# Kernel optimization log

Hardware: AMD Instinct MI355X
Metric: run time of the kernel (lower is better)

The kernel has to match this reference:

```python
import jax, jax.numpy as jnp
import numpy as np

B, N, IN_DIM, HIDDEN, N_CLASS = 32768, 25, 3, 128, 2

# BODY_25 skeleton edges from the repo
_SRC = np.array([17, 15, 18, 16, 0, 2, 3, 4, 5, 6, 7, 8, 9, 12, 10, 13, 11, 14, 23, 22, 24, 20, 19, 21])
_DST = np.array([15, 0, 16, 0, 1, 1, 2, 3, 1, 5, 6, 1, 8, 8, 9, 12, 10, 13, 22, 11, 11, 19, 14, 14])


def setup_inputs() -> dict:
    key = jax.random.key(0)
    ks = jax.random.split(key, 4)
    # skeleton edges + self loops (dgl.add_self_loop)
    src = jnp.asarray(np.concatenate([_SRC, np.arange(N)]), dtype=jnp.int64)
    dst = jnp.asarray(np.concatenate([_DST, np.arange(N)]), dtype=jnp.int64)
    return {
        "x": jax.random.normal(ks[0], (B, N, IN_DIM), dtype=jnp.float32),
        "src": src,
        "dst": dst,
        "W1": jax.random.normal(ks[1], (IN_DIM, HIDDEN), dtype=jnp.float32) / np.sqrt(IN_DIM),
        "b1": jnp.zeros((HIDDEN,), jnp.float32),
        "W2": jax.random.normal(ks[2], (HIDDEN, HIDDEN), dtype=jnp.float32) / np.sqrt(HIDDEN),
        "b2": jnp.zeros((HIDDEN,), jnp.float32),
        "Wfc": jax.random.normal(ks[3], (HIDDEN, N_CLASS), dtype=jnp.float32) / np.sqrt(HIDDEN),
        "bfc": jnp.zeros((N_CLASS,), jnp.float32),
    }


def reference(x, src, dst, W1, b1, W2, b2, Wfc, bfc):
    # x: [B, N, F] node features for B identical-topology skeleton graphs
    Bn, Nn, _ = x.shape
    ones = jnp.ones(src.shape, x.dtype)
    deg_out = jax.ops.segment_sum(ones, src, num_segments=Nn)  # [N]
    deg_in = jax.ops.segment_sum(ones, dst, num_segments=Nn)   # [N]
    # DGL GraphConv norm='both': D_in^{-1/2} A D_out^{-1/2} X W + b
    cs = jnp.where(deg_out > 0, deg_out ** -0.5, 0.0)
    ci = jnp.where(deg_in > 0, deg_in ** -0.5, 0.0)

    def gconv(h, W, b):
        msg = h[:, src, :] * cs[src][None, :, None]            # gather + src norm
        agg = jnp.zeros_like(h).at[:, dst, :].add(msg)          # scatter-add
        agg = agg * ci[None, :, None]                           # dst norm
        return agg @ W + b

    h = jax.nn.relu(gconv(x, W1, b1))
    h = jax.nn.relu(gconv(h, W2, b2))
    pooled = jnp.mean(h, axis=1)  # dgl.mean_nodes -> [B, HIDDEN]
    return pooled @ Wfc + bfc      # [B, N_CLASS]
```

## Files before the change

kernel.cpp:

```cpp
#include <hip/hip_runtime.h>

#define NN    25
#define FIN   3
#define HID   128
#define GPB   4
#define ROWDW 64

typedef int i32x4 __attribute__((ext_vector_type(4)));
typedef unsigned int uint;

static __device__ __forceinline__ long pack8(const int* q)
{
    unsigned long v = 0;
    #pragma unroll
    for (int j = 0; j < 8; ++j)
        v |= ((unsigned long)(unsigned char)(q[j] & 255)) << (8 * j);
    return (long)v;
}

__global__ void pack_w2_i8(const float* __restrict__ W2, float* __restrict__ scales,
                           long* __restrict__ w2q)
{
    __shared__ float red[4];
    const int tid = threadIdx.x;

    float m = 1e-20f;
    #pragma unroll
    for (int i = 0; i < (HID * HID) / 256; ++i)
        m = fmaxf(m, fabsf(W2[i * 256 + tid]));
    #pragma unroll
    for (int off = 32; off > 0; off >>= 1)
        m = fmaxf(m, __shfl_xor(m, off));
    if ((tid & 63) == 0) red[tid >> 6] = m;
    __syncthreads();
    const float bmax = fmaxf(fmaxf(red[0], red[1]), fmaxf(red[2], red[3]));
    const float Sb = 32000.0f / bmax;
    if (blockIdx.x == 0 && tid == 0) { scales[0] = bmax; scales[1] = Sb; }

    int gi = blockIdx.x * 256 + tid;
    int l  = gi & 63;
    int nt = (gi >> 6) & 7;
    int kt = (gi >> 9) & 3;
    int p  = gi >> 11;
    int n  = nt * 16 + (l & 15);
    int kb = kt * 32 + (l >> 4) * 8;
    int q8[8];
    #pragma unroll
    for (int j = 0; j < 8; ++j) {
        int qv = (int)rintf(W2[(kb + j) * HID + n] * Sb);
        qv = min(max(qv, -32600), 32600);
        int lo = ((qv + 128) & 255) - 128;
        int hi = (qv - lo) >> 8;
        q8[j] = p ? lo : hi;
    }
    w2q[gi] = pack8(q8);
}

static __device__ __forceinline__ void agg25_inplace(float2* A)
{
    const float cA = 0.40824829f;
    const float cB = 0.31622777f;
    const float cC = 0.44721360f;
    const float cH = 0.5f;
    const float cS = 0.70710678f;
    A[1]  = cB * (A[0] + A[2] + A[5] + A[8]) + cC * A[1];
    A[0]  = cA * (A[15] + A[16] + A[0]);
    A[2]  = cH * (A[3]  + A[2]);
    A[3]  = cH * (A[4]  + A[3]);
    A[4]  = cS *  A[4];
    A[5]  = cH * (A[6]  + A[5]);
    A[6]  = cH * (A[7]  + A[6]);
    A[7]  = cS *  A[7];
    A[8]  = cA * (A[9] + A[12] + A[8]);
    A[9]  = cH * (A[10] + A[9]);
    A[10] = cH * (A[11] + A[10]);
    A[11] = cA * (A[22] + A[24] + A[11]);
    A[12] = cH * (A[13] + A[12]);
    A[13] = cH * (A[14] + A[13]);
    A[14] = cA * (A[19] + A[21] + A[14]);
    A[15] = cH * (A[17] + A[15]);
    A[16] = cH * (A[18] + A[16]);
    A[17] = cS *  A[17];
    A[18] = cS *  A[18];
    A[19] = cH * (A[20] + A[19]);
    A[20] = cS *  A[20];
    A[21] = cS *  A[21];
    A[22] = cH * (A[23] + A[22]);
    A[23] = cS *  A[23];
    A[24] = cS *  A[24];
}

static __device__ __forceinline__ void unpack16(uint4 d, long& hi, long& lo)
{
    uint h01 = __builtin_amdgcn_perm(d.y, d.x, 0x07050301u) ^ 0x80808080u;
    uint h23 = __builtin_amdgcn_perm(d.w, d.z, 0x07050301u) ^ 0x80808080u;
    uint l01 = __builtin_amdgcn_perm(d.y, d.x, 0x06040200u) ^ 0x80808080u;
    uint l23 = __builtin_amdgcn_perm(d.w, d.z, 0x06040200u) ^ 0x80808080u;
    uint hv[2] = {h01, h23};
    uint lv[2] = {l01, l23};
    __builtin_memcpy(&hi, hv, 8);
    __builtin_memcpy(&lo, lv, 8);
}

__global__ __launch_bounds__(256, 5) void gcn_main(
    const float* __restrict__ x,
    const float* __restrict__ W1, const float* __restrict__ b1,
    const float* __restrict__ b2,
    const float* __restrict__ Wfc, const float* __restrict__ bfc,
    const long* __restrict__ w2q, const float* __restrict__ scales,
    float* __restrict__ out)
{
    __shared__ __align__(16) uint bufQ[GPB][NN * ROWDW];

    const int tid  = threadIdx.x;
    const int w    = tid >> 6;
    const int lane = tid & 63;
    const int g    = blockIdx.x * GPB + w;
    const int c0   = lane * 2;
    const int m0   = lane & 15;
    const int quad = lane >> 4;

    const float Sb = scales[1];
    float msk1[4];
    #pragma unroll
    for (int rr = 0; rr < 4; ++rr)
        msk1[rr] = (quad * 4 + rr < 9) ? 1.0f : 0.0f;

    float* xsw = (float*)bufQ[w];
    const float* xg = x + (size_t)g * (NN * FIN);
    xsw[lane] = xg[lane];
    if (lane < NN * FIN - 64) xsw[64 + lane] = xg[64 + lane];
    asm volatile("s_waitcnt lgkmcnt(0)" ::: "memory");

    float2 w1r0 = *(const float2*)(W1 + 0 * HID + c0);
    float2 w1r1 = *(const float2*)(W1 + 1 * HID + c0);
    float2 w1r2 = *(const float2*)(W1 + 2 * HID + c0);
    float2 A[NN];
    const float4* xv = (const float4*)bufQ[w];
    #pragma unroll
    for (int grp = 0; grp < 6; ++grp) {
        float4 p = xv[grp * 3 + 0];
        float4 q = xv[grp * 3 + 1];
        float4 r = xv[grp * 3 + 2];
        float xa[4][3] = {{p.x, p.y, p.z}, {p.w, q.x, q.y},
                          {q.z, q.w, r.x}, {r.y, r.z, r.w}};
        #pragma unroll
        for (int j = 0; j < 4; ++j) {
            int n = grp * 4 + j;
            A[n].x = fmaf(xa[j][0], w1r0.x, fmaf(xa[j][1], w1r1.x, xa[j][2] * w1r2.x));
            A[n].y = fmaf(xa[j][0], w1r0.y, fmaf(xa[j][1], w1r1.y, xa[j][2] * w1r2.y));
        }
    }
    {
        float x0 = xsw[72], x1 = xsw[73], x2 = xsw[74];
        A[24].x = fmaf(x0, w1r0.x, fmaf(x1, w1r1.x, x2 * w1r2.x));
        A[24].y = fmaf(x0, w1r0.y, fmaf(x1, w1r1.y, x2 * w1r2.y));
    }

    float2 b1v = *(const float2*)(b1 + c0);
    agg25_inplace(A);
    #pragma unroll
    for (int n = 0; n < NN; ++n) {
        A[n].x = fmaxf(A[n].x + b1v.x, 0.0f);
        A[n].y = fmaxf(A[n].y + b1v.y, 0.0f);
    }

    agg25_inplace(A);

    float am = 1e-20f;
    #pragma unroll
    for (int n = 0; n < NN; ++n)
        am = fmaxf(am, fmaxf(fabsf(A[n].x), fabsf(A[n].y)));
    #pragma unroll
    for (int off = 32; off > 0; off >>= 1)
        am = fmaxf(am, __shfl_xor(am, off));
    const float Sa = 32000.0f / am;

    const float invRs = Sa * Sb * (1.0f / 256.0f);
    int b2q[8];
    #pragma unroll
    for (int t = 0; t < 8; ++t)
        b2q[t] = (int)rintf(b2[t * 16 + m0] * invRs);

    asm volatile("" ::: "memory");
    const int blk = lane >> 2;
    const int sub = lane & 3;
    #pragma unroll
    for (int n = 0; n < NN; ++n) {
        uint qx = (uint)fmaf(A[n].x, Sa, 32896.5f);
        uint qy = (uint)fmaf(A[n].y, Sa, 32896.5f);
        int col = ((blk ^ (n & 15)) << 2) | sub;
        bufQ[w][(n << 6) + col] = __builtin_amdgcn_perm(qy, qx, 0x05040100u);
    }
    asm volatile("s_waitcnt lgkmcnt(0)" ::: "memory");

    const int m1 = min(16 + m0, NN - 1);

    long ah[2][4], al[2][4];
    #pragma unroll
    for (int kt = 0; kt < 4; ++kt) {
        int b = (kt << 2) | quad;
        uint4 d0 = *(const uint4*)&bufQ[w][(m0 << 6) + ((b ^ m0) << 2)];
        uint4 d1 = *(const uint4*)&bufQ[w][(m1 << 6) + ((b ^ (m1 & 15)) << 2)];
        unpack16(d0, ah[0][kt], al[0][kt]);
        unpack16(d1, ah[1][kt], al[1][kt]);
    }

    const float rsL = 256.0f / (Sa * Sb);

    float s0 = 0.0f, s1 = 0.0f;
    #pragma unroll
    for (int nt = 0; nt < 8; ++nt) {
        float2 wfc = *(const float2*)(Wfc + (nt * 16 + m0) * 2);

        i32x4 aHH[2], aX[2];
        i32x4 bi;
        bi[0] = b2q[nt]; bi[1] = b2q[nt]; bi[2] = b2q[nt]; bi[3] = b2q[nt];
        aHH[0] = (i32x4)0; aHH[1] = (i32x4)0;
        aX[0] = bi; aX[1] = bi;

        #pragma unroll
        for (int kt = 0; kt < 4; ++kt) {
            long bh = w2q[(size_t)(((0 + kt) * 8 + nt) * 64 + lane)];
            long bl = w2q[(size_t)(((4 + kt) * 8 + nt) * 64 + lane)];
            aHH[0] = __builtin_amdgcn_mfma_i32_16x16x32_i8(ah[0][kt], bh, aHH[0], 0, 0, 0);
            aHH[1] = __builtin_amdgcn_mfma_i32_16x16x32_i8(ah[1][kt], bh, aHH[1], 0, 0, 0);
            aX[0]  = __builtin_amdgcn_mfma_i32_16x16x32_i8(ah[0][kt], bl, aX[0], 0, 0, 0);
            aX[0]  = __builtin_amdgcn_mfma_i32_16x16x32_i8(al[0][kt], bh, aX[0], 0, 0, 0);
            aX[1]  = __builtin_amdgcn_mfma_i32_16x16x32_i8(ah[1][kt], bl, aX[1], 0, 0, 0);
            aX[1]  = __builtin_amdgcn_mfma_i32_16x16x32_i8(al[1][kt], bh, aX[1], 0, 0, 0);
        }

        float s = 0.0f;
        #pragma unroll
        for (int rr = 0; rr < 4; ++rr) {
            int ci = (int)(((uint)aHH[0][rr] << 8)) + aX[0][rr];
            s += (float)max(ci, 0);
        }
        #pragma unroll
        for (int rr = 0; rr < 4; ++rr) {
            int ci = (int)(((uint)aHH[1][rr] << 8)) + aX[1][rr];
            s = fmaf((float)max(ci, 0), msk1[rr], s);
        }
        s0 = fmaf(s, wfc.x, s0);
        s1 = fmaf(s, wfc.y, s1);
    }

    #pragma unroll
    for (int off = 32; off > 0; off >>= 1) {
        s0 += __shfl_down(s0, off);
        s1 += __shfl_down(s1, off);
    }
    if (lane == 0) {
        const float post = rsL * (1.0f / 25.0f);
        out[g * 2 + 0] = fmaf(s0, post, bfc[0]);
        out[g * 2 + 1] = fmaf(s1, post, bfc[1]);
    }
}

extern "C" void kernel_launch(void* const* d_in, const int* in_sizes, int n_in,
                              void* d_out, int out_size, void* d_ws, size_t ws_size,
                              hipStream_t stream)
{
    const float* x   = (const float*)d_in[0];
    const float* W1  = (const float*)d_in[3];
    const float* b1  = (const float*)d_in[4];
    const float* W2  = (const float*)d_in[5];
    const float* b2  = (const float*)d_in[6];
    const float* Wfc = (const float*)d_in[7];
    const float* bfc = (const float*)d_in[8];
    float* out = (float*)d_out;

    const int Btot = in_sizes[0] / (NN * FIN);

    float* scales = (float*)d_ws;
    long*  w2q    = (long*)((char*)d_ws + 256);

    hipLaunchKernelGGL(pack_w2_i8, dim3(16), dim3(256), 0, stream, W2, scales, w2q);
    hipLaunchKernelGGL(gcn_main, dim3(Btot / GPB), dim3(256), 0, stream,
                       x, W1, b1, b2, Wfc, bfc, w2q, scales, out);
}
```

Baseline: 166.1 us.

## Switch int8 W2 GEMM from 16x16x32 to 32x32x16 MFMA tiles

Repacks the quantized W2 into the 32x32x16 i8 MFMA operand layout and recomputes the layer-2 GEMM with 32-row tiles. The 25 nodes now fit in one padded 32-row tile instead of two 16-row tiles, which cuts the MFMA count from 48 to 24 per wave per output tile. Padded rows are zeroed, and their bias-only contribution is subtracted analytically. Row sums are kept in integer form, and launch bounds occupancy drops from 5 to 4 to make room for the larger accumulator registers. Int32 summation of 16 values may risk overflow, and occupancy is lower.

```diff
diff --git a/kernel.cpp b/kernel.cpp
--- a/kernel.cpp
+++ b/kernel.cpp
@@ -6,7 +6,7 @@
 #define GPB   4
 #define ROWDW 64
 
-typedef int i32x4 __attribute__((ext_vector_type(4)));
+typedef int i32x16 __attribute__((ext_vector_type(16)));
 typedef unsigned int uint;
 
 static __device__ __forceinline__ long pack8(const int* q)
@@ -39,11 +39,11 @@
 
     int gi = blockIdx.x * 256 + tid;
     int l  = gi & 63;
-    int nt = (gi >> 6) & 7;
-    int kt = (gi >> 9) & 3;
-    int p  = gi >> 11;
-    int n  = nt * 16 + (l & 15);
-    int kb = kt * 32 + (l >> 4) * 8;
+    int nt = (gi >> 6) & 3;
+    int kt = (gi >> 8) & 7;
+    int p  = (gi >> 11) & 1;
+    int n  = nt * 32 + (l & 31);
+    int kb = kt * 16 + (l >> 5) * 8;
     int q8[8];
     #pragma unroll
     for (int j = 0; j < 8; ++j) {
@@ -102,7 +102,7 @@
     __builtin_memcpy(&lo, lv, 8);
 }
 
-__global__ __launch_bounds__(256, 5) void gcn_main(
+__global__ __launch_bounds__(256, 4) void gcn_main(
     const float* __restrict__ x,
     const float* __restrict__ W1, const float* __restrict__ b1,
     const float* __restrict__ b2,
@@ -117,14 +117,10 @@
     const int lane = tid & 63;
     const int g    = blockIdx.x * GPB + w;
     const int c0   = lane * 2;
-    const int m0   = lane & 15;
-    const int quad = lane >> 4;
+    const int col  = lane & 31;
+    const int half = lane >> 5;
 
     const float Sb = scales[1];
-    float msk1[4];
-    #pragma unroll
-    for (int rr = 0; rr < 4; ++rr)
-        msk1[rr] = (quad * 4 + rr < 9) ? 1.0f : 0.0f;
 
     float* xsw = (float*)bufQ[w];
     const float* xg = x + (size_t)g * (NN * FIN);
@@ -177,10 +173,10 @@
     const float Sa = 32000.0f / am;
 
     const float invRs = Sa * Sb * (1.0f / 256.0f);
-    int b2q[8];
-    #pragma unroll
-    for (int t = 0; t < 8; ++t)
-        b2q[t] = (int)rintf(b2[t * 16 + m0] * invRs);
+    int b2q[4];
+    #pragma unroll
+    for (int t = 0; t < 4; ++t)
+        b2q[t] = (int)rintf(b2[t * 32 + col] * invRs);
 
     asm volatile("" ::: "memory");
     const int blk = lane >> 2;
@@ -189,61 +185,54 @@
     for (int n = 0; n < NN; ++n) {
         uint qx = (uint)fmaf(A[n].x, Sa, 32896.5f);
         uint qy = (uint)fmaf(A[n].y, Sa, 32896.5f);
-        int col = ((blk ^ (n & 15)) << 2) | sub;
-        bufQ[w][(n << 6) + col] = __builtin_amdgcn_perm(qy, qx, 0x05040100u);
+        int cw = ((blk ^ (n & 15)) << 2) | sub;
+        bufQ[w][(n << 6) + cw] = __builtin_amdgcn_perm(qy, qx, 0x05040100u);
     }
     asm volatile("s_waitcnt lgkmcnt(0)" ::: "memory");
 
-    const int m1 = min(16 + m0, NN - 1);
-
-    long ah[2][4], al[2][4];
-    #pragma unroll
-    for (int kt = 0; kt < 4; ++kt) {
-        int b = (kt << 2) | quad;
-        uint4 d0 = *(const uint4*)&bufQ[w][(m0 << 6) + ((b ^ m0) << 2)];
-        uint4 d1 = *(const uint4*)&bufQ[w][(m1 << 6) + ((b ^ (m1 & 15)) << 2)];
-        unpack16(d0, ah[0][kt], al[0][kt]);
-        unpack16(d1, ah[1][kt], al[1][kt]);
-    }
-
-    const float rsL = 256.0f / (Sa * Sb);
+    const int arow = col > 24 ? 24 : col;
+    long ah[8], al[8];
+    #pragma unroll
+    for (int kt = 0; kt < 8; ++kt) {
+        int b = (kt << 1) | half;
+        uint4 d = *(const uint4*)&bufQ[w][(arow << 6) + ((b ^ (arow & 15)) << 2)];
+        unpack16(d, ah[kt], al[kt]);
+    }
+    if (col > 24) {
+        #pragma unroll
+        for (int kt = 0; kt < 8; ++kt) { ah[kt] = 0; al[kt] = 0; }
+    }
+
+    const float rsL  = 256.0f / (Sa * Sb);
+    const int   nInv = 3 + half;
 
     float s0 = 0.0f, s1 = 0.0f;
     #pragma unroll
-    for (int nt = 0; nt < 8; ++nt) {
-        float2 wfc = *(const float2*)(Wfc + (nt * 16 + m0) * 2);
-
-        i32x4 aHH[2], aX[2];
-        i32x4 bi;
-        bi[0] = b2q[nt]; bi[1] = b2q[nt]; bi[2] = b2q[nt]; bi[3] = b2q[nt];
-        aHH[0] = (i32x4)0; aHH[1] = (i32x4)0;
-        aX[0] = bi; aX[1] = bi;
-
-        #pragma unroll
-        for (int kt = 0; kt < 4; ++kt) {
-            long bh = w2q[(size_t)(((0 + kt) * 8 + nt) * 64 + lane)];
-            long bl = w2q[(size_t)(((4 + kt) * 8 + nt) * 64 + lane)];
-            aHH[0] = __builtin_amdgcn_mfma_i32_16x16x32_i8(ah[0][kt], bh, aHH[0], 0, 0, 0);
-            aHH[1] = __builtin_amdgcn_mfma_i32_16x16x32_i8(ah[1][kt], bh, aHH[1], 0, 0, 0);
-            aX[0]  = __builtin_amdgcn_mfma_i32_16x16x32_i8(ah[0][kt], bl, aX[0], 0, 0, 0);
-            aX[0]  = __builtin_amdgcn_mfma_i32_16x16x32_i8(al[0][kt], bh, aX[0], 0, 0, 0);
-            aX[1]  = __builtin_amdgcn_mfma_i32_16x16x32_i8(ah[1][kt], bl, aX[1], 0, 0, 0);
-            aX[1]  = __builtin_amdgcn_mfma_i32_16x16x32_i8(al[1][kt], bh, aX[1], 0, 0, 0);
+    for (int nt = 0; nt < 4; ++nt) {
+        float2 wfc = *(const float2*)(Wfc + (nt * 32 + col) * 2);
+
+        i32x16 aHH = (i32x16)0;
+        i32x16 aX  = (i32x16)b2q[nt];
+
+        #pragma unroll
+        for (int kt = 0; kt < 8; ++kt) {
+            long bh = w2q[(size_t)(((0 + kt) * 4 + nt) * 64 + lane)];
+            long bl = w2q[(size_t)(((8 + kt) * 4 + nt) * 64 + lane)];
+            aHH = __builtin_amdgcn_mfma_i32_32x32x16_i8(ah[kt], bh, aHH, 0, 0, 0);
+            aX  = __builtin_amdgcn_mfma_i32_32x32x16_i8(ah[kt], bl, aX, 0, 0, 0);
+            aX  = __builtin_amdgcn_mfma_i32_32x32x16_i8(al[kt], bh, aX, 0, 0, 0);
         }
 
-        float s = 0.0f;
-        #pragma unroll
-        for (int rr = 0; rr < 4; ++rr) {
-            int ci = (int)(((uint)aHH[0][rr] << 8)) + aX[0][rr];
-            s += (float)max(ci, 0);
+        int si = 0;
+        #pragma unroll
+        for (int r = 0; r < 16; ++r) {
+            int ci = (int)(((uint)aHH[r]) << 8) + aX[r];
+            si += max(ci, 0);
         }
-        #pragma unroll
-        for (int rr = 0; rr < 4; ++rr) {
-            int ci = (int)(((uint)aHH[1][rr] << 8)) + aX[1][rr];
-            s = fmaf((float)max(ci, 0), msk1[rr], s);
-        }
-        s0 = fmaf(s, wfc.x, s0);
-        s1 = fmaf(s, wfc.y, s1);
+        si -= nInv * max(b2q[nt], 0);
+        float sf = (float)si;
+        s0 = fmaf(sf, wfc.x, s0);
+        s1 = fmaf(sf, wfc.y, s1);
     }
 
     #pragma unroll
```

Result: slower. 173.3 us (+4.3%).
